# Kernel optimization log

Hardware: AMD Instinct MI355X
Metric: run time of the kernel (lower is better)

The kernel has to match this reference:

```python
import jax, jax.numpy as jnp
import numpy as np

B, N = 4, 1024
DIM, DEPTH, HEADS, DIM_HEAD, TCD = 512, 4, 8, 64, 512
HID = HEADS * DIM_HEAD  # 512
INNER = 4 * DIM         # 2048
MAX_REL = 32
N_REL = 2 * MAX_REL + 1  # 65
SCALE = DIM_HEAD ** -0.5
EPS = 1e-5


def setup_inputs() -> dict:
    key = jax.random.key(0)
    ks = jax.random.split(key, 16)
    s = 0.02
    inp = {
        "x": jax.random.normal(ks[0], (B, N, DIM), jnp.float32),
        "time": jax.random.normal(ks[1], (B, 1, TCD), jnp.float32),
        "seq_mask": jnp.ones((B, N), jnp.float32),
        "residue_index": jnp.tile(jnp.arange(N, dtype=jnp.int32)[None], (B, 1)),
        # relative positional encoding linear (65 -> heads)
        "relpos_w": jax.random.normal(ks[2], (N_REL, HEADS), jnp.float32) * s,
        "relpos_b": jnp.zeros((HEADS,), jnp.float32),
        # per-layer attention params (stacked over depth)
        "attn_norm_g": jnp.ones((DEPTH, DIM), jnp.float32),
        "attn_time_w": jax.random.normal(ks[3], (DEPTH, TCD, 2 * DIM), jnp.float32) * s,
        "attn_time_b": jnp.zeros((DEPTH, 2 * DIM), jnp.float32),
        "to_q_w": jax.random.normal(ks[4], (DEPTH, DIM, HID), jnp.float32) * s,
        "to_kv_w": jax.random.normal(ks[5], (DEPTH, DIM, 2 * HID), jnp.float32) * s,
        "to_out_w": jax.random.normal(ks[6], (DEPTH, HID, DIM), jnp.float32) * s,
        # per-layer feedforward params
        "ff_norm_g": jnp.ones((DEPTH, DIM), jnp.float32),
        "ff_time_w": jax.random.normal(ks[7], (DEPTH, TCD, 2 * INNER), jnp.float32) * s,
        "ff_time_b": jnp.zeros((DEPTH, 2 * INNER), jnp.float32),
        "ff_in_w": jax.random.normal(ks[8], (DEPTH, DIM, INNER), jnp.float32) * s,
        "ff_in_b": jnp.zeros((DEPTH, INNER), jnp.float32),
        "ff_out_w": jax.random.normal(ks[9], (DEPTH, INNER, DIM), jnp.float32) * s,
        "ff_out_b": jnp.zeros((DEPTH, DIM), jnp.float32),
    }
    return inp


def _ln(x, g):
    m = jnp.mean(x, axis=-1, keepdims=True)
    v = jnp.mean(jnp.square(x - m), axis=-1, keepdims=True)
    return (x - m) * jax.lax.rsqrt(v + EPS) * g


def _forward(x, time, seq_mask, residue_index, relpos_w, relpos_b,
             attn_norm_g, attn_time_w, attn_time_b, to_q_w, to_kv_w, to_out_w,
             ff_norm_g, ff_time_w, ff_time_b, ff_in_w, ff_in_b, ff_out_w, ff_out_b):
    # relative positional bias: [b, heads, i, j]
    d_ij = residue_index[:, :, None] - residue_index[:, None, :]
    idx = jnp.clip(d_ij, -MAX_REL, MAX_REL) + MAX_REL  # argmin over integer bins == clip
    bias = relpos_w[idx] + relpos_b                    # [b, i, j, h]
    bias = jnp.transpose(bias, (0, 3, 1, 2))           # [b, h, i, j]

    mask3 = seq_mask[..., None]                                       # [b, n, 1]
    pair_mask = seq_mask[:, None, :, None] * seq_mask[:, None, None, :]  # [b, 1, i, j]
    t_act = jax.nn.silu(time)                                         # [b, 1, tcd]

    x = x * mask3
    for d in range(DEPTH):
        # ---- attention block ----
        sc_sh = t_act @ attn_time_w[d] + attn_time_b[d]               # [b, 1, 2*dim]
        sc, sh = jnp.split(sc_sh, 2, axis=-1)
        xn = _ln(x, attn_norm_g[d]) * (sc + 1.0) + sh
        xn = xn * mask3
        q = (xn @ to_q_w[d]).reshape(B, N, HEADS, DIM_HEAD) * SCALE
        # NOTE: context = pre-norm x (faithful to original code)
        kv = (x @ to_kv_w[d]).reshape(B, N, 2, HEADS, DIM_HEAD)
        k, v = kv[:, :, 0], kv[:, :, 1]
        sim = jnp.einsum('bihd,bjhd->bhij', q, k) + bias
        sim = sim - (1.0 - pair_mask) * 1e6
        attn = jax.nn.softmax(sim, axis=-1)
        out = jnp.einsum('bhij,bjhd->bihd', attn, v).reshape(B, N, HID)
        out = (out @ to_out_w[d]) * mask3
        x = x + out
        # ---- feedforward block ----
        sc_sh = t_act @ ff_time_w[d] + ff_time_b[d]                   # [b, 1, 2*inner]
        sc, sh = jnp.split(sc_sh, 2, axis=-1)
        h = jax.nn.silu(_ln(x, ff_norm_g[d]) @ ff_in_w[d] + ff_in_b[d])
        h = h * (sc + 1.0) + sh
        x = x + (h @ ff_out_w[d] + ff_out_b[d])
        x = x * mask3
    return x


def reference(x, time, seq_mask, residue_index, relpos_w, relpos_b,
              attn_norm_g, attn_time_w, attn_time_b, to_q_w, to_kv_w, to_out_w,
              ff_norm_g, ff_time_w, ff_time_b, ff_in_w, ff_in_b, ff_out_w, ff_out_b):
    return _forward(x, time, seq_mask, residue_index, relpos_w, relpos_b,
                    attn_norm_g, attn_time_w, attn_time_b, to_q_w, to_kv_w, to_out_w,
                    ff_norm_g, ff_time_w, ff_time_b, ff_in_w, ff_in_b, ff_out_w, ff_out_b)
```

## Files before the change

kernel.cpp:

```cpp
#include <hip/hip_runtime.h>
#include <hip/hip_bf16.h>

constexpr int kB = 4, kN = 1024, kD = 512, kH = 8, kDh = 64, kT = 512;
constexpr int kHid = 512, kI = 2048, kRel = 65, kDepth = 4;
constexpr int kBN = kB * kN;

typedef short s16x8 __attribute__((ext_vector_type(8)));
typedef float f32x4 __attribute__((ext_vector_type(4)));

__device__ __forceinline__ float ldin(const void* p, long i, int isb) {
  if (isb) return __bfloat162float(((const __hip_bfloat16*)p)[i]);
  return ((const float*)p)[i];
}

__device__ __forceinline__ unsigned short bfbits(float v) {
  __hip_bfloat16 h = __float2bfloat16(v);
  return *(unsigned short*)&h;
}

__device__ __forceinline__ void gload16(const void* g, void* l) {
  __builtin_amdgcn_global_load_lds(
      (const __attribute__((address_space(1))) unsigned int*)g,
      (__attribute__((address_space(3))) unsigned int*)l, 16, 0, 0);
}

__global__ void k_detect(const void* __restrict__ x, int* __restrict__ flag) {
  const unsigned int* u = (const unsigned int*)x;
  unsigned int v = u[threadIdx.x];
  int e = (v >> 7) & 0xFF;
  int good = (e >= 100 && e <= 140) ? 1 : 0;
  unsigned long long m = __ballot(good);
  if (threadIdx.x == 0) flag[0] = (__popcll(m) >= 48) ? 1 : 0;
}

__global__ void k_xinit(const void* __restrict__ xin, const void* __restrict__ seqm,
                        float* __restrict__ x, __hip_bfloat16* __restrict__ xb,
                        const int* __restrict__ flag) {
  const int isb = *flag;
  const long base = ((long)blockIdx.x * 256 + threadIdx.x) * 8;
  const int row = (int)(base >> 9);
  const float mk = ldin(seqm, row, isb);
  __align__(16) unsigned short pk[8];
  #pragma unroll
  for (int j = 0; j < 8; j++) {
    float v = ldin(xin, base + j, isb) * mk;
    x[base + j] = v;
    pk[j] = bfbits(v);
  }
  *(uint4*)(xb + base) = *(const uint4*)pk;
}

__global__ __launch_bounds__(256) void k_timeproj_part(
    const void* __restrict__ timein,
    const void* __restrict__ atw, const void* __restrict__ ftw,
    float* __restrict__ part, const int* __restrict__ flag) {
  const int isb = *flag;
  __shared__ float T[kB * 64];
  const int d = blockIdx.z, kc = blockIdx.y;
  const int tt0 = kc * 64;
  {
    const int b = threadIdx.x >> 6, ttl = threadIdx.x & 63;
    const float tv = ldin(timein, (long)b * kT + tt0 + ttl, isb);
    T[b * 64 + ttl] = tv / (1.f + __expf(-tv));
  }
  __syncthreads();
  const int c = blockIdx.x * 256 + threadIdx.x;
  float a0 = 0, a1 = 0, a2 = 0, a3 = 0;
  if (c < 2 * kD) {
    const long wo = (long)d * kT * 2 * kD + (long)tt0 * 2 * kD + c;
    #pragma unroll 4
    for (int tt = 0; tt < 64; tt++) {
      const float w = ldin(atw, wo + (long)tt * 2 * kD, isb);
      a0 += T[0 * 64 + tt] * w; a1 += T[1 * 64 + tt] * w;
      a2 += T[2 * 64 + tt] * w; a3 += T[3 * 64 + tt] * w;
    }
  } else {
    const int c2 = c - 2 * kD;
    const long wo = (long)d * kT * 2 * kI + (long)tt0 * 2 * kI + c2;
    #pragma unroll 4
    for (int tt = 0; tt < 64; tt++) {
      const float w = ldin(ftw, wo + (long)tt * 2 * kI, isb);
      a0 += T[0 * 64 + tt] * w; a1 += T[1 * 64 + tt] * w;
      a2 += T[2 * 64 + tt] * w; a3 += T[3 * 64 + tt] * w;
    }
  }
  float* pp = part + ((long)(d * 8 + kc) * 4) * 5120 + c;
  pp[0] = a0; pp[5120] = a1; pp[2 * 5120] = a2; pp[3 * 5120] = a3;
}

__global__ __launch_bounds__(256) void k_timeproj_comb(
    const float* __restrict__ part,
    const void* __restrict__ atb, const void* __restrict__ ftb,
    float* __restrict__ ascsh, float* __restrict__ fscsh,
    const int* __restrict__ flag) {
  const int isb = *flag;
  const int d = blockIdx.y;
  const int c = blockIdx.x * 256 + threadIdx.x;
  float s[4] = {0, 0, 0, 0};
  #pragma unroll
  for (int kc = 0; kc < 8; kc++) {
    const float* pp = part + ((long)(d * 8 + kc) * 4) * 5120 + c;
    s[0] += pp[0]; s[1] += pp[5120]; s[2] += pp[2 * 5120]; s[3] += pp[3 * 5120];
  }
  if (c < 2 * kD) {
    const float bv = ldin(atb, (long)d * 2 * kD + c, isb);
    #pragma unroll
    for (int b = 0; b < 4; b++) ascsh[((long)d * kB + b) * 2 * kD + c] = s[b] + bv;
  } else {
    const int c2 = c - 2 * kD;
    const float bv = ldin(ftb, (long)d * 2 * kI + c2, isb);
    #pragma unroll
    for (int b = 0; b < 4; b++) fscsh[((long)d * kB + b) * 2 * kI + c2] = s[b] + bv;
  }
}

__global__ __launch_bounds__(256) void k_wtall(
    const void* __restrict__ wq, const void* __restrict__ wkv,
    const void* __restrict__ wo, const void* __restrict__ wfi,
    const void* __restrict__ wfo,
    __hip_bfloat16* __restrict__ wtq, __hip_bfloat16* __restrict__ wtkv,
    __hip_bfloat16* __restrict__ wto, __hip_bfloat16* __restrict__ wtfi,
    __hip_bfloat16* __restrict__ wtfo, const int* __restrict__ flag) {
  const int isb = *flag;
  __shared__ float T[64][65];
  const int bx = blockIdx.x;
  const void* W; __hip_bfloat16* Wt; int K, N, tl;
  if (bx < 256)       { W = wq;  Wt = wtq;  K = 512;  N = 512;  tl = bx; }
  else if (bx < 768)  { W = wkv; Wt = wtkv; K = 512;  N = 1024; tl = bx - 256; }
  else if (bx < 1024) { W = wo;  Wt = wto;  K = 512;  N = 512;  tl = bx - 768; }
  else if (bx < 2048) { W = wfi; Wt = wtfi; K = 512;  N = 2048; tl = bx - 1024; }
  else                { W = wfo; Wt = wtfo; K = 2048; N = 512;  tl = bx - 2048; }
  const int nx = N >> 6, nk = K >> 6;
  const int z = tl / (nx * nk);
  const int rem = tl % (nx * nk);
  const int k0 = (rem / nx) * 64, n0 = (rem % nx) * 64;
  const long ibase = (long)z * K * N;
  const long obase = (long)z * N * K;
  const int t = threadIdx.x;
  const int cn = t & 63, r4 = t >> 6;
  for (int rr = r4; rr < 64; rr += 4)
    T[rr][cn] = ldin(W, ibase + (long)(k0 + rr) * N + n0 + cn, isb);
  __syncthreads();
  for (int nn = r4; nn < 64; nn += 4)
    Wt[obase + (long)(n0 + nn) * K + k0 + cn] = __float2bfloat16(T[cn][nn]);
}

__global__ __launch_bounds__(256) void k_ln(
    const float* __restrict__ x, const void* __restrict__ g,
    const float* __restrict__ scsh, const void* __restrict__ seqm,
    __hip_bfloat16* __restrict__ xnb, int d, int domod, const int* __restrict__ flag) {
  const int isb = *flag;
  const int wid = threadIdx.x >> 6, lane = threadIdx.x & 63;
  const int row = blockIdx.x * 4 + wid;
  const int b = row >> 10;
  const float* xr = x + (long)row * kD + lane * 8;
  const float4 v0 = *(const float4*)xr;
  const float4 v1 = *(const float4*)(xr + 4);
  float v[8] = {v0.x, v0.y, v0.z, v0.w, v1.x, v1.y, v1.z, v1.w};
  float s = 0.f, s2 = 0.f;
  #pragma unroll
  for (int i = 0; i < 8; i++) { s += v[i]; s2 += v[i] * v[i]; }
  #pragma unroll
  for (int off = 1; off < 64; off <<= 1) { s += __shfl_xor(s, off); s2 += __shfl_xor(s2, off); }
  const float mean = s * (1.f / kD);
  const float var = fmaxf(s2 * (1.f / kD) - mean * mean, 0.f);
  const float rstd = rsqrtf(var + 1e-5f);
  float mk = 1.f;
  if (domod) mk = ldin(seqm, row, isb);
  __align__(16) unsigned short pk[8];
  #pragma unroll
  for (int i = 0; i < 8; i++) {
    const int cc = lane * 8 + i;
    float y = (v[i] - mean) * rstd * ldin(g, (long)d * kD + cc, isb);
    if (domod)
      y = (y * (scsh[(long)b * 2 * kD + cc] + 1.f) + scsh[(long)b * 2 * kD + kD + cc]) * mk;
    pk[i] = bfbits(y);
  }
  *(uint4*)(xnb + (long)row * kD + lane * 8) = *(const uint4*)pk;
}

template <int EPI, int BN>
__global__ __launch_bounds__(256) void k_mgemm(
    const __hip_bfloat16* __restrict__ A, const __hip_bfloat16* __restrict__ Wt,
    long woff, int K, int Nc,
    __hip_bfloat16* __restrict__ Cb,
    float* __restrict__ X, __hip_bfloat16* __restrict__ Xb,
    const void* __restrict__ bias, long boff,
    const float* __restrict__ scsh, const void* __restrict__ seqm,
    const int* __restrict__ flag) {
  constexpr int FN = BN / 32;
  const int isb = *flag;
  __shared__ __align__(16) short As[2][64 * 64];
  __shared__ __align__(16) short Bs[2][BN * 64];
  const int t = threadIdx.x;
  const int l = t & 63, wid = t >> 6;
  const int wm = wid & 1, wn = wid >> 1;
  const int lr = l >> 4, lc = l & 15;
  const int m0 = blockIdx.y * 64, n0 = blockIdx.x * BN;

  f32x4 acc[2][FN] = {};
  const int lrow8 = l >> 3;
  const int lchunk = (l & 7) ^ lrow8;
  const __hip_bfloat16* gA = A + (long)(m0 + wid * 8 + lrow8) * K + lchunk * 8;
  const __hip_bfloat16* gB = Wt + woff + (long)(n0 + wid * 8 + lrow8) * K + lchunk * 8;

  #pragma unroll
  for (int p = 0; p < 2; p++)
    gload16(gA + (long)p * 32 * K, &As[0][p * 2048 + wid * 512]);
  #pragma unroll
  for (int p = 0; p < FN; p++)
    gload16(gB + (long)p * 32 * K, &Bs[0][p * 2048 + wid * 512]);
  __syncthreads();

  const int nt = K >> 6;
  int cur = 0;
  for (int tt = 0; tt < nt; tt++) {
    if (tt + 1 < nt) {
      const int k0 = (tt + 1) * 64;
      #pragma unroll
      for (int p = 0; p < 2; p++)
        gload16(gA + (long)p * 32 * K + k0, &As[cur ^ 1][p * 2048 + wid * 512]);
      #pragma unroll
      for (int p = 0; p < FN; p++)
        gload16(gB + (long)p * 32 * K + k0, &Bs[cur ^ 1][p * 2048 + wid * 512]);
    }
    #pragma unroll
    for (int kk = 0; kk < 2; kk++) {
      s16x8 af[2], bf[FN];
      #pragma unroll
      for (int fm = 0; fm < 2; fm++) {
        const int r = wm * 32 + fm * 16 + lc;
        af[fm] = *(const s16x8*)&As[cur][r * 64 + (((kk * 4 + lr) ^ (r & 7)) * 8)];
      }
      #pragma unroll
      for (int fn = 0; fn < FN; fn++) {
        const int r = wn * (BN / 2) + fn * 16 + lc;
        bf[fn] = *(const s16x8*)&Bs[cur][r * 64 + (((kk * 4 + lr) ^ (r & 7)) * 8)];
      }
      #pragma unroll
      for (int fm = 0; fm < 2; fm++)
        #pragma unroll
        for (int fn = 0; fn < FN; fn++)
          acc[fm][fn] = __builtin_amdgcn_mfma_f32_16x16x32_bf16(af[fm], bf[fn], acc[fm][fn], 0, 0, 0);
    }
    __syncthreads();
    cur ^= 1;
  }

  #pragma unroll
  for (int fm = 0; fm < 2; fm++) {
    #pragma unroll
    for (int j = 0; j < 4; j++) {
      const int r = m0 + wm * 32 + fm * 16 + lr * 4 + j;
      const int bb = r >> 10;
      float mk = 1.f;
      if constexpr (EPI == 2 || EPI == 4) mk = ldin(seqm, r, isb);
      #pragma unroll
      for (int fn = 0; fn < FN; fn++) {
        const int cc = n0 + wn * (BN / 2) + fn * 16 + lc;
        const long off = (long)r * Nc + cc;
        float v = acc[fm][fn][j];
        if constexpr (EPI == 2) {
          X[off] += v * mk;
        } else if constexpr (EPI == 3) {
          v += ldin(bias, boff + cc, isb);
          v = v / (1.f + __expf(-v));
          v = v * (scsh[(long)bb * 2 * kI + cc] + 1.f) + scsh[(long)bb * 2 * kI + kI + cc];
          Cb[off] = __float2bfloat16(v);
        } else {
          v += ldin(bias, boff + cc, isb);
          const float nx = (X[off] + v) * mk;
          X[off] = nx;
          Xb[off] = __float2bfloat16(nx);
        }
      }
    }
  }
}

__global__ __launch_bounds__(256) void k_qkv(
    const __hip_bfloat16* __restrict__ xnb, const __hip_bfloat16* __restrict__ xb,
    const __hip_bfloat16* __restrict__ wtq, const __hip_bfloat16* __restrict__ wtkv,
    __hip_bfloat16* __restrict__ qbuf, __hip_bfloat16* __restrict__ kvb) {
  constexpr int K = kD;
  __shared__ __align__(16) short As[2][64 * 64];
  __shared__ __align__(16) short Bs[2][128 * 64];
  const int t = threadIdx.x;
  const int l = t & 63, wid = t >> 6;
  const int wm = wid & 1, wn = wid >> 1;
  const int lr = l >> 4, lc = l & 15;
  const int m0 = blockIdx.y * 64;

  const __hip_bfloat16* A; const __hip_bfloat16* Wt; __hip_bfloat16* C;
  int Nc, n0; float scale;
  if (blockIdx.x < 4) {
    A = xnb; Wt = wtq; C = qbuf; Nc = kHid; n0 = blockIdx.x * 128; scale = 0.125f;
  } else {
    A = xb; Wt = wtkv; C = kvb; Nc = 2 * kHid; n0 = (blockIdx.x - 4) * 128; scale = 1.f;
  }

  f32x4 acc[2][4] = {};
  const int lrow8 = l >> 3;
  const int lchunk = (l & 7) ^ lrow8;
  const __hip_bfloat16* gA = A + (long)(m0 + wid * 8 + lrow8) * K + lchunk * 8;
  const __hip_bfloat16* gB = Wt + (long)(n0 + wid * 8 + lrow8) * K + lchunk * 8;

  #pragma unroll
  for (int p = 0; p < 2; p++)
    gload16(gA + (long)p * 32 * K, &As[0][p * 2048 + wid * 512]);
  #pragma unroll
  for (int p = 0; p < 4; p++)
    gload16(gB + (long)p * 32 * K, &Bs[0][p * 2048 + wid * 512]);
  __syncthreads();

  const int nt = K >> 6;
  int cur = 0;
  for (int tt = 0; tt < nt; tt++) {
    if (tt + 1 < nt) {
      const int k0 = (tt + 1) * 64;
      #pragma unroll
      for (int p = 0; p < 2; p++)
        gload16(gA + (long)p * 32 * K + k0, &As[cur ^ 1][p * 2048 + wid * 512]);
      #pragma unroll
      for (int p = 0; p < 4; p++)
        gload16(gB + (long)p * 32 * K + k0, &Bs[cur ^ 1][p * 2048 + wid * 512]);
    }
    #pragma unroll
    for (int kk = 0; kk < 2; kk++) {
      s16x8 af[2], bf[4];
      #pragma unroll
      for (int fm = 0; fm < 2; fm++) {
        const int r = wm * 32 + fm * 16 + lc;
        af[fm] = *(const s16x8*)&As[cur][r * 64 + (((kk * 4 + lr) ^ (r & 7)) * 8)];
      }
      #pragma unroll
      for (int fn = 0; fn < 4; fn++) {
        const int r = wn * 64 + fn * 16 + lc;
        bf[fn] = *(const s16x8*)&Bs[cur][r * 64 + (((kk * 4 + lr) ^ (r & 7)) * 8)];
      }
      #pragma unroll
      for (int fm = 0; fm < 2; fm++)
        #pragma unroll
        for (int fn = 0; fn < 4; fn++)
          acc[fm][fn] = __builtin_amdgcn_mfma_f32_16x16x32_bf16(af[fm], bf[fn], acc[fm][fn], 0, 0, 0);
    }
    __syncthreads();
    cur ^= 1;
  }

  #pragma unroll
  for (int fm = 0; fm < 2; fm++)
    #pragma unroll
    for (int j = 0; j < 4; j++) {
      const int r = m0 + wm * 32 + fm * 16 + lr * 4 + j;
      #pragma unroll
      for (int fn = 0; fn < 4; fn++) {
        const int cc = n0 + wn * 64 + fn * 16 + lc;
        C[(long)r * Nc + cc] = __float2bfloat16(acc[fm][fn][j] * scale);
      }
    }
}

__global__ __launch_bounds__(256) void k_attn(
    const __hip_bfloat16* __restrict__ qb, const __hip_bfloat16* __restrict__ kvb,
    __hip_bfloat16* __restrict__ aob,
    const void* __restrict__ rpw, const void* __restrict__ rpb,
    const void* __restrict__ seqm, const int* __restrict__ ridx,
    const int* __restrict__ flag) {
  const int isb = *flag;
  const int t = threadIdx.x;
  const int bid = blockIdx.x;
  const int swz = (bid & 7) * 64 + (bid >> 3);
  const int x = swz & 15, h = (swz >> 4) & 7, b = swz >> 7;
  const int i0 = x * 64;

  __shared__ __align__(16) short Ks[2][64 * 64];
  __shared__ __align__(16) short Vt[2][64 * 72];
  __shared__ __align__(16) short Ps[4][16 * 72];
  __shared__ float biasw[kRel];
  __shared__ int riq[64];
  __shared__ float mkq[64];
  __shared__ int rik[2][64];
  __shared__ float mkk[2][64];

  const int l = t & 63, wid = t >> 6;
  const int g = l >> 4, li = l & 15;

  if (t < kRel) biasw[t] = ldin(rpw, (long)t * kH + h, isb) + ldin(rpb, h, isb);
  if (t < 64) { riq[t] = ridx[b * kN + i0 + t]; mkq[t] = ldin(seqm, b * kN + i0 + t, isb); }

  const __hip_bfloat16* qptr =
      qb + ((long)(b * kN + i0 + wid * 16 + li)) * kHid + h * kDh + g * 8;
  s16x8 aq[2];
  aq[0] = *(const s16x8*)qptr;
  aq[1] = *(const s16x8*)(qptr + 32);

  {
    #pragma unroll
    for (int p = 0; p < 2; p++) {
      const int j = p * 32 + wid * 8 + (l >> 3);
      const short* gk = (const short*)kvb + ((long)(b * kN + j)) * 1024 + h * 64 +
                        (((l & 7) ^ (l >> 3)) * 8);
      gload16(gk, &Ks[0][p * 2048 + wid * 512]);
    }
    const short* gv = (const short*)kvb + ((long)(b * kN + l)) * 1024 + 512 + h * 64 + wid * 16;
    s16x8 v0 = *(const s16x8*)gv;
    s16x8 v1 = *(const s16x8*)(gv + 8);
    #pragma unroll
    for (int dd = 0; dd < 8; dd++) {
      Vt[0][(wid * 16 + dd) * 72 + l] = v0[dd];
      Vt[0][(wid * 16 + 8 + dd) * 72 + l] = v1[dd];
    }
    if (t < 64) { rik[0][t] = ridx[b * kN + t]; mkk[0][t] = ldin(seqm, b * kN + t, isb); }
  }
  __syncthreads();

  float mkqv[4]; int riqv[4];
  #pragma unroll
  for (int r = 0; r < 4; r++) {
    riqv[r] = riq[wid * 16 + g * 4 + r];
    mkqv[r] = mkq[wid * 16 + g * 4 + r];
  }

  float m_run[4] = {-1e30f, -1e30f, -1e30f, -1e30f};
  float l_run[4] = {0.f, 0.f, 0.f, 0.f};
  f32x4 o[4] = {};

  constexpr int NT = kN / 64;
  int cur = 0;
  for (int tt = 0; tt < NT; tt++) {
    s16x8 nv0, nv1;
    int nri = 0; float nmk = 0.f;
    const bool have = (tt + 1) < NT;
    if (have) {
      const int j0n = (tt + 1) * 64;
      #pragma unroll
      for (int p = 0; p < 2; p++) {
        const int j = p * 32 + wid * 8 + (l >> 3);
        const short* gk = (const short*)kvb + ((long)(b * kN + j0n + j)) * 1024 + h * 64 +
                          (((l & 7) ^ (l >> 3)) * 8);
        gload16(gk, &Ks[cur ^ 1][p * 2048 + wid * 512]);
      }
      const short* gv =
          (const short*)kvb + ((long)(b * kN + j0n + l)) * 1024 + 512 + h * 64 + wid * 16;
      nv0 = *(const s16x8*)gv;
      nv1 = *(const s16x8*)(gv + 8);
      if (t < 64) { nri = ridx[b * kN + j0n + t]; nmk = ldin(seqm, b * kN + j0n + t, isb); }
    }

    f32x4 s[4] = {};
    __builtin_amdgcn_s_setprio(1);
    #pragma unroll
    for (int kc = 0; kc < 2; kc++) {
      #pragma unroll
      for (int fc = 0; fc < 4; fc++) {
        const int jl = fc * 16 + li;
        const s16x8 bk = *(const s16x8*)&Ks[cur][jl * 64 + ((kc * 32 + g * 8) ^ ((li & 7) * 8))];
        s[fc] = __builtin_amdgcn_mfma_f32_16x16x32_bf16(aq[kc], bk, s[fc], 0, 0, 0);
      }
    }
    __builtin_amdgcn_s_setprio(0);

    int rikv[4]; float mkkv[4];
    #pragma unroll
    for (int fc = 0; fc < 4; fc++) {
      rikv[fc] = rik[cur][fc * 16 + li];
      mkkv[fc] = mkk[cur][fc * 16 + li];
    }
    #pragma unroll
    for (int fc = 0; fc < 4; fc++) {
      #pragma unroll
      for (int r = 0; r < 4; r++) {
        int di = riqv[r] - rikv[fc];
        di = di < -32 ? -32 : (di > 32 ? 32 : di);
        s[fc][r] += biasw[di + 32] - (1.f - mkqv[r] * mkkv[fc]) * 1e6f;
      }
    }

    #pragma unroll
    for (int r = 0; r < 4; r++) {
      float mx = fmaxf(fmaxf(s[0][r], s[1][r]), fmaxf(s[2][r], s[3][r]));
      mx = fmaxf(mx, __shfl_xor(mx, 1));
      mx = fmaxf(mx, __shfl_xor(mx, 2));
      mx = fmaxf(mx, __shfl_xor(mx, 4));
      mx = fmaxf(mx, __shfl_xor(mx, 8));
      const float m_new = fmaxf(m_run[r], mx);
      const float e = __expf(m_run[r] - m_new);
      float ps = 0.f;
      #pragma unroll
      for (int fc = 0; fc < 4; fc++) {
        const float p = __expf(s[fc][r] - m_new);
        ps += p;
        Ps[wid][(g * 4 + r) * 72 + fc * 16 + li] = (short)bfbits(p);
      }
      ps += __shfl_xor(ps, 1);
      ps += __shfl_xor(ps, 2);
      ps += __shfl_xor(ps, 4);
      ps += __shfl_xor(ps, 8);
      l_run[r] = l_run[r] * e + ps;
      m_run[r] = m_new;
      o[0][r] *= e; o[1][r] *= e; o[2][r] *= e; o[3][r] *= e;
    }

    __builtin_amdgcn_s_setprio(1);
    #pragma unroll
    for (int kc = 0; kc < 2; kc++) {
      const s16x8 pa = *(const s16x8*)&Ps[wid][li * 72 + kc * 32 + g * 8];
      #pragma unroll
      for (int fd = 0; fd < 4; fd++) {
        const s16x8 bv = *(const s16x8*)&Vt[cur][(fd * 16 + li) * 72 + kc * 32 + g * 8];
        o[fd] = __builtin_amdgcn_mfma_f32_16x16x32_bf16(pa, bv, o[fd], 0, 0, 0);
      }
    }
    __builtin_amdgcn_s_setprio(0);

    if (have) {
      #pragma unroll
      for (int dd = 0; dd < 8; dd++) {
        Vt[cur ^ 1][(wid * 16 + dd) * 72 + l] = nv0[dd];
        Vt[cur ^ 1][(wid * 16 + 8 + dd) * 72 + l] = nv1[dd];
      }
      if (t < 64) { rik[cur ^ 1][t] = nri; mkk[cur ^ 1][t] = nmk; }
    }
    __syncthreads();
    cur ^= 1;
  }

  float inv[4];
  #pragma unroll
  for (int r = 0; r < 4; r++) inv[r] = 1.f / l_run[r];
  #pragma unroll
  for (int fd = 0; fd < 4; fd++) {
    #pragma unroll
    for (int r = 0; r < 4; r++) {
      const long off =
          ((long)(b * kN + i0 + wid * 16 + g * 4 + r)) * kHid + h * kDh + fd * 16 + li;
      aob[off] = __float2bfloat16(o[fd][r] * inv[r]);
    }
  }
}

__global__ void k_out(const float* __restrict__ x, void* __restrict__ out,
                      const int* __restrict__ flag) {
  const int i = blockIdx.x * 256 + threadIdx.x;
  if (*flag) ((__hip_bfloat16*)out)[i] = __float2bfloat16(x[i]);
  else ((float*)out)[i] = x[i];
}

extern "C" void kernel_launch(void* const* d_in, const int* in_sizes, int n_in,
                              void* d_out, int out_size, void* d_ws, size_t ws_size,
                              hipStream_t stream) {
  const void* xin  = d_in[0];
  const void* timein = d_in[1];
  const void* seqm = d_in[2];
  const int*  ridx = (const int*)d_in[3];
  const void* rpw  = d_in[4];
  const void* rpb  = d_in[5];
  const void* ang  = d_in[6];
  const void* atw  = d_in[7];
  const void* atb  = d_in[8];
  const void* wq   = d_in[9];
  const void* wkv  = d_in[10];
  const void* wo   = d_in[11];
  const void* fng  = d_in[12];
  const void* ftw  = d_in[13];
  const void* ftb  = d_in[14];
  const void* wfi  = d_in[15];
  const void* bfi  = d_in[16];
  const void* wfo  = d_in[17];
  const void* bfo  = d_in[18];

  float* ws = (float*)d_ws;
  float* x     = ws;
  float* ascsh = ws + 2097152;
  float* fscsh = ws + 2113536;
  float* part  = ws + 2179072;
  int*   flag  = (int*)(ws + 2834432);
  __hip_bfloat16* bfb = (__hip_bfloat16*)(ws + 2834496);
  __hip_bfloat16* xnb  = bfb;
  __hip_bfloat16* xb   = bfb + 2097152;
  __hip_bfloat16* aob  = bfb + 4194304;
  __hip_bfloat16* hb   = bfb + 6291456;
  __hip_bfloat16* qbuf = bfb + 14680064;
  __hip_bfloat16* kvb  = bfb + 16777216;
  __hip_bfloat16* wtq  = bfb + 20971520;
  __hip_bfloat16* wtkv = bfb + 22020096;
  __hip_bfloat16* wto  = bfb + 24117248;
  __hip_bfloat16* wtfi = bfb + 25165824;
  __hip_bfloat16* wtfo = bfb + 29360128;

  k_detect<<<1, 64, 0, stream>>>(xin, flag);
  k_xinit<<<kBN * kD / 2048, 256, 0, stream>>>(xin, seqm, x, xb, flag);
  k_timeproj_part<<<dim3(20, 8, kDepth), 256, 0, stream>>>(timein, atw, ftw, part, flag);
  k_timeproj_comb<<<dim3(20, kDepth), 256, 0, stream>>>(part, atb, ftb, ascsh, fscsh, flag);
  k_wtall<<<3072, 256, 0, stream>>>(wq, wkv, wo, wfi, wfo, wtq, wtkv, wto, wtfi, wtfo, flag);

  for (int d = 0; d < kDepth; ++d) {
    k_ln<<<kBN / 4, 256, 0, stream>>>(x, ang, ascsh + (long)d * kB * 2 * kD, seqm, xnb, d, 1, flag);
    k_qkv<<<dim3(12, kBN / 64), 256, 0, stream>>>(
        xnb, xb, wtq + (long)d * kD * kHid, wtkv + (long)d * kD * 2 * kHid, qbuf, kvb);
    k_attn<<<512, 256, 0, stream>>>(qbuf, kvb, aob, rpw, rpb, seqm, ridx, flag);
    k_mgemm<2, 64><<<dim3(kD / 64, kBN / 64), 256, 0, stream>>>(
        aob, wto, (long)d * kHid * kD, kHid, kD, nullptr, x, nullptr,
        nullptr, 0, nullptr, seqm, flag);
    k_ln<<<kBN / 4, 256, 0, stream>>>(x, fng, nullptr, seqm, xnb, d, 0, flag);
    k_mgemm<3, 128><<<dim3(kI / 128, kBN / 64), 256, 0, stream>>>(
        xnb, wtfi, (long)d * kD * kI, kD, kI, hb, nullptr, nullptr,
        bfi, (long)d * kI, fscsh + (long)d * kB * 2 * kI, nullptr, flag);
    k_mgemm<4, 64><<<dim3(kD / 64, kBN / 64), 256, 0, stream>>>(
        hb, wtfo, (long)d * kI * kD, kI, kD, nullptr, x, xb,
        bfo, (long)d * kD, nullptr, seqm, flag);
  }
  k_out<<<kBN * kD / 256, 256, 0, stream>>>(x, d_out, flag);
}
```

Before: 792.3 us.

## Split attention over key halves with a combine kernel, shrink GEMM tiles

```diff
diff --git a/kernel.cpp b/kernel.cpp
--- a/kernel.cpp
+++ b/kernel.cpp
@@ -284,7 +284,7 @@
     __hip_bfloat16* __restrict__ qbuf, __hip_bfloat16* __restrict__ kvb) {
   constexpr int K = kD;
   __shared__ __align__(16) short As[2][64 * 64];
-  __shared__ __align__(16) short Bs[2][128 * 64];
+  __shared__ __align__(16) short Bs[2][64 * 64];
   const int t = threadIdx.x;
   const int l = t & 63, wid = t >> 6;
   const int wm = wid & 1, wn = wid >> 1;
@@ -293,24 +293,23 @@
 
   const __hip_bfloat16* A; const __hip_bfloat16* Wt; __hip_bfloat16* C;
   int Nc, n0; float scale;
-  if (blockIdx.x < 4) {
-    A = xnb; Wt = wtq; C = qbuf; Nc = kHid; n0 = blockIdx.x * 128; scale = 0.125f;
+  if (blockIdx.x < 8) {
+    A = xnb; Wt = wtq; C = qbuf; Nc = kHid; n0 = blockIdx.x * 64; scale = 0.125f;
   } else {
-    A = xb; Wt = wtkv; C = kvb; Nc = 2 * kHid; n0 = (blockIdx.x - 4) * 128; scale = 1.f;
-  }
-
-  f32x4 acc[2][4] = {};
+    A = xb; Wt = wtkv; C = kvb; Nc = 2 * kHid; n0 = (blockIdx.x - 8) * 64; scale = 1.f;
+  }
+
+  f32x4 acc[2][2] = {};
   const int lrow8 = l >> 3;
   const int lchunk = (l & 7) ^ lrow8;
   const __hip_bfloat16* gA = A + (long)(m0 + wid * 8 + lrow8) * K + lchunk * 8;
   const __hip_bfloat16* gB = Wt + (long)(n0 + wid * 8 + lrow8) * K + lchunk * 8;
 
   #pragma unroll
-  for (int p = 0; p < 2; p++)
+  for (int p = 0; p < 2; p++) {
     gload16(gA + (long)p * 32 * K, &As[0][p * 2048 + wid * 512]);
-  #pragma unroll
-  for (int p = 0; p < 4; p++)
     gload16(gB + (long)p * 32 * K, &Bs[0][p * 2048 + wid * 512]);
+  }
   __syncthreads();
 
   const int nt = K >> 6;
@@ -319,29 +318,28 @@
     if (tt + 1 < nt) {
       const int k0 = (tt + 1) * 64;
       #pragma unroll
-      for (int p = 0; p < 2; p++)
+      for (int p = 0; p < 2; p++) {
         gload16(gA + (long)p * 32 * K + k0, &As[cur ^ 1][p * 2048 + wid * 512]);
-      #pragma unroll
-      for (int p = 0; p < 4; p++)
         gload16(gB + (long)p * 32 * K + k0, &Bs[cur ^ 1][p * 2048 + wid * 512]);
+      }
     }
     #pragma unroll
     for (int kk = 0; kk < 2; kk++) {
-      s16x8 af[2], bf[4];
+      s16x8 af[2], bf[2];
       #pragma unroll
       for (int fm = 0; fm < 2; fm++) {
         const int r = wm * 32 + fm * 16 + lc;
         af[fm] = *(const s16x8*)&As[cur][r * 64 + (((kk * 4 + lr) ^ (r & 7)) * 8)];
       }
       #pragma unroll
-      for (int fn = 0; fn < 4; fn++) {
-        const int r = wn * 64 + fn * 16 + lc;
+      for (int fn = 0; fn < 2; fn++) {
+        const int r = wn * 32 + fn * 16 + lc;
         bf[fn] = *(const s16x8*)&Bs[cur][r * 64 + (((kk * 4 + lr) ^ (r & 7)) * 8)];
       }
       #pragma unroll
       for (int fm = 0; fm < 2; fm++)
         #pragma unroll
-        for (int fn = 0; fn < 4; fn++)
+        for (int fn = 0; fn < 2; fn++)
           acc[fm][fn] = __builtin_amdgcn_mfma_f32_16x16x32_bf16(af[fm], bf[fn], acc[fm][fn], 0, 0, 0);
     }
     __syncthreads();
@@ -354,16 +352,16 @@
     for (int j = 0; j < 4; j++) {
       const int r = m0 + wm * 32 + fm * 16 + lr * 4 + j;
       #pragma unroll
-      for (int fn = 0; fn < 4; fn++) {
-        const int cc = n0 + wn * 64 + fn * 16 + lc;
+      for (int fn = 0; fn < 2; fn++) {
+        const int cc = n0 + wn * 32 + fn * 16 + lc;
         C[(long)r * Nc + cc] = __float2bfloat16(acc[fm][fn][j] * scale);
       }
     }
 }
 
-__global__ __launch_bounds__(256) void k_attn(
+__global__ __launch_bounds__(512) void k_attn(
     const __hip_bfloat16* __restrict__ qb, const __hip_bfloat16* __restrict__ kvb,
-    __hip_bfloat16* __restrict__ aob,
+    float* __restrict__ opart, float* __restrict__ mpart, float* __restrict__ lpart,
     const void* __restrict__ rpw, const void* __restrict__ rpb,
     const void* __restrict__ seqm, const int* __restrict__ ridx,
     const int* __restrict__ flag) {
@@ -371,15 +369,16 @@
   const int t = threadIdx.x;
   const int bid = blockIdx.x;
   const int swz = (bid & 7) * 64 + (bid >> 3);
-  const int x = swz & 15, h = (swz >> 4) & 7, b = swz >> 7;
-  const int i0 = x * 64;
+  const int jh = swz & 1, x = (swz >> 1) & 7, h = (swz >> 4) & 7, b = swz >> 7;
+  const int i0 = x * 128;
+  const int jbase = jh * 512;
 
   __shared__ __align__(16) short Ks[2][64 * 64];
   __shared__ __align__(16) short Vt[2][64 * 72];
-  __shared__ __align__(16) short Ps[4][16 * 72];
+  __shared__ __align__(16) short Ps[8][16 * 72];
   __shared__ float biasw[kRel];
-  __shared__ int riq[64];
-  __shared__ float mkq[64];
+  __shared__ int riq[128];
+  __shared__ float mkq[128];
   __shared__ int rik[2][64];
   __shared__ float mkk[2][64];
 
@@ -387,7 +386,7 @@
   const int g = l >> 4, li = l & 15;
 
   if (t < kRel) biasw[t] = ldin(rpw, (long)t * kH + h, isb) + ldin(rpb, h, isb);
-  if (t < 64) { riq[t] = ridx[b * kN + i0 + t]; mkq[t] = ldin(seqm, b * kN + i0 + t, isb); }
+  if (t < 128) { riq[t] = ridx[b * kN + i0 + t]; mkq[t] = ldin(seqm, b * kN + i0 + t, isb); }
 
   const __hip_bfloat16* qptr =
       qb + ((long)(b * kN + i0 + wid * 16 + li)) * kHid + h * kDh + g * 8;
@@ -396,22 +395,19 @@
   aq[1] = *(const s16x8*)(qptr + 32);
 
   {
-    #pragma unroll
-    for (int p = 0; p < 2; p++) {
-      const int j = p * 32 + wid * 8 + (l >> 3);
-      const short* gk = (const short*)kvb + ((long)(b * kN + j)) * 1024 + h * 64 +
-                        (((l & 7) ^ (l >> 3)) * 8);
-      gload16(gk, &Ks[0][p * 2048 + wid * 512]);
-    }
-    const short* gv = (const short*)kvb + ((long)(b * kN + l)) * 1024 + 512 + h * 64 + wid * 16;
+    const int j = wid * 8 + (l >> 3);
+    const short* gk = (const short*)kvb + ((long)(b * kN + jbase + j)) * 1024 + h * 64 +
+                      (((l & 7) ^ (l >> 3)) * 8);
+    gload16(gk, &Ks[0][wid * 512]);
+    const short* gv =
+        (const short*)kvb + ((long)(b * kN + jbase + l)) * 1024 + 512 + h * 64 + wid * 8;
     s16x8 v0 = *(const s16x8*)gv;
-    s16x8 v1 = *(const s16x8*)(gv + 8);
-    #pragma unroll
-    for (int dd = 0; dd < 8; dd++) {
-      Vt[0][(wid * 16 + dd) * 72 + l] = v0[dd];
-      Vt[0][(wid * 16 + 8 + dd) * 72 + l] = v1[dd];
-    }
-    if (t < 64) { rik[0][t] = ridx[b * kN + t]; mkk[0][t] = ldin(seqm, b * kN + t, isb); }
+    #pragma unroll
+    for (int dd = 0; dd < 8; dd++) Vt[0][(wid * 8 + dd) * 72 + l] = v0[dd];
+    if (t < 64) {
+      rik[0][t] = ridx[b * kN + jbase + t];
+      mkk[0][t] = ldin(seqm, b * kN + jbase + t, isb);
+    }
   }
   __syncthreads();
 
@@ -426,25 +422,21 @@
   float l_run[4] = {0.f, 0.f, 0.f, 0.f};
   f32x4 o[4] = {};
 
-  constexpr int NT = kN / 64;
+  constexpr int NT = 8;
   int cur = 0;
   for (int tt = 0; tt < NT; tt++) {
-    s16x8 nv0, nv1;
+    s16x8 nv0;
     int nri = 0; float nmk = 0.f;
     const bool have = (tt + 1) < NT;
     if (have) {
-      const int j0n = (tt + 1) * 64;
-      #pragma unroll
-      for (int p = 0; p < 2; p++) {
-        const int j = p * 32 + wid * 8 + (l >> 3);
-        const short* gk = (const short*)kvb + ((long)(b * kN + j0n + j)) * 1024 + h * 64 +
-                          (((l & 7) ^ (l >> 3)) * 8);
-        gload16(gk, &Ks[cur ^ 1][p * 2048 + wid * 512]);
-      }
+      const int j0n = jbase + (tt + 1) * 64;
+      const int j = wid * 8 + (l >> 3);
+      const short* gk = (const short*)kvb + ((long)(b * kN + j0n + j)) * 1024 + h * 64 +
+                        (((l & 7) ^ (l >> 3)) * 8);
+      gload16(gk, &Ks[cur ^ 1][wid * 512]);
       const short* gv =
-          (const short*)kvb + ((long)(b * kN + j0n + l)) * 1024 + 512 + h * 64 + wid * 16;
+          (const short*)kvb + ((long)(b * kN + j0n + l)) * 1024 + 512 + h * 64 + wid * 8;
       nv0 = *(const s16x8*)gv;
-      nv1 = *(const s16x8*)(gv + 8);
       if (t < 64) { nri = ridx[b * kN + j0n + t]; nmk = ldin(seqm, b * kN + j0n + t, isb); }
     }
 
@@ -516,28 +508,60 @@
 
     if (have) {
       #pragma unroll
-      for (int dd = 0; dd < 8; dd++) {
-        Vt[cur ^ 1][(wid * 16 + dd) * 72 + l] = nv0[dd];
-        Vt[cur ^ 1][(wid * 16 + 8 + dd) * 72 + l] = nv1[dd];
-      }
+      for (int dd = 0; dd < 8; dd++) Vt[cur ^ 1][(wid * 8 + dd) * 72 + l] = nv0[dd];
       if (t < 64) { rik[cur ^ 1][t] = nri; mkk[cur ^ 1][t] = nmk; }
     }
     __syncthreads();
     cur ^= 1;
   }
 
-  float inv[4];
-  #pragma unroll
-  for (int r = 0; r < 4; r++) inv[r] = 1.f / l_run[r];
   #pragma unroll
   for (int fd = 0; fd < 4; fd++) {
     #pragma unroll
     for (int r = 0; r < 4; r++) {
       const long off =
           ((long)(b * kN + i0 + wid * 16 + g * 4 + r)) * kHid + h * kDh + fd * 16 + li;
-      aob[off] = __float2bfloat16(o[fd][r] * inv[r]);
-    }
-  }
+      opart[(long)jh * 2097152 + off] = o[fd][r];
+    }
+  }
+  if (li == 0) {
+    #pragma unroll
+    for (int r = 0; r < 4; r++) {
+      const int row = i0 + wid * 16 + g * 4 + r;
+      const int idx = (b * kN + row) * 8 + h;
+      mpart[jh * 32768 + idx] = m_run[r];
+      lpart[jh * 32768 + idx] = l_run[r];
+    }
+  }
+}
+
+__global__ __launch_bounds__(256) void k_acomb(
+    const float* __restrict__ opart, const float* __restrict__ mpart,
+    const float* __restrict__ lpart, __hip_bfloat16* __restrict__ aob) {
+  const long e = ((long)blockIdx.x * 256 + threadIdx.x) * 8;
+  const int h = (int)((e >> 6) & 7);
+  const int row = (int)(e >> 9);
+  const int idx = row * 8 + h;
+  const float m0 = mpart[idx], m1 = mpart[32768 + idx];
+  const float l0 = lpart[idx], l1 = lpart[32768 + idx];
+  const float mm = fmaxf(m0, m1);
+  const float e0 = __expf(m0 - mm), e1 = __expf(m1 - mm);
+  const float den = fmaxf(e0 * l0 + e1 * l1, 1e-30f);
+  const float s0 = e0 / den, s1 = e1 / den;
+  const float4 a0 = *(const float4*)(opart + e);
+  const float4 a1 = *(const float4*)(opart + e + 4);
+  const float4 b0 = *(const float4*)(opart + 2097152 + e);
+  const float4 b1 = *(const float4*)(opart + 2097152 + e + 4);
+  __align__(16) unsigned short pk[8];
+  pk[0] = bfbits(a0.x * s0 + b0.x * s1);
+  pk[1] = bfbits(a0.y * s0 + b0.y * s1);
+  pk[2] = bfbits(a0.z * s0 + b0.z * s1);
+  pk[3] = bfbits(a0.w * s0 + b0.w * s1);
+  pk[4] = bfbits(a1.x * s0 + b1.x * s1);
+  pk[5] = bfbits(a1.y * s0 + b1.y * s1);
+  pk[6] = bfbits(a1.z * s0 + b1.z * s1);
+  pk[7] = bfbits(a1.w * s0 + b1.w * s1);
+  *(uint4*)(aob + e) = *(const uint4*)pk;
 }
 
 __global__ void k_out(const float* __restrict__ x, void* __restrict__ out,
@@ -588,6 +612,9 @@
   __hip_bfloat16* wto  = bfb + 24117248;
   __hip_bfloat16* wtfi = bfb + 25165824;
   __hip_bfloat16* wtfo = bfb + 29360128;
+  float* opart = (float*)hb;
+  float* mpart = part;
+  float* lpart = part + 65536;
 
   k_detect<<<1, 64, 0, stream>>>(xin, flag);
   k_xinit<<<kBN * kD / 2048, 256, 0, stream>>>(xin, seqm, x, xb, flag);
@@ -597,14 +624,15 @@
 
   for (int d = 0; d < kDepth; ++d) {
     k_ln<<<kBN / 4, 256, 0, stream>>>(x, ang, ascsh + (long)d * kB * 2 * kD, seqm, xnb, d, 1, flag);
-    k_qkv<<<dim3(12, kBN / 64), 256, 0, stream>>>(
+    k_qkv<<<dim3(24, kBN / 64), 256, 0, stream>>>(
         xnb, xb, wtq + (long)d * kD * kHid, wtkv + (long)d * kD * 2 * kHid, qbuf, kvb);
-    k_attn<<<512, 256, 0, stream>>>(qbuf, kvb, aob, rpw, rpb, seqm, ridx, flag);
+    k_attn<<<512, 512, 0, stream>>>(qbuf, kvb, opart, mpart, lpart, rpw, rpb, seqm, ridx, flag);
+    k_acomb<<<1024, 256, 0, stream>>>(opart, mpart, lpart, aob);
     k_mgemm<2, 64><<<dim3(kD / 64, kBN / 64), 256, 0, stream>>>(
         aob, wto, (long)d * kHid * kD, kHid, kD, nullptr, x, nullptr,
         nullptr, 0, nullptr, seqm, flag);
     k_ln<<<kBN / 4, 256, 0, stream>>>(x, fng, nullptr, seqm, xnb, d, 0, flag);
-    k_mgemm<3, 128><<<dim3(kI / 128, kBN / 64), 256, 0, stream>>>(
+    k_mgemm<3, 64><<<dim3(kI / 64, kBN / 64), 256, 0, stream>>>(
         xnb, wtfi, (long)d * kD * kI, kD, kI, hb, nullptr, nullptr,
         bfi, (long)d * kI, fscsh + (long)d * kB * 2 * kI, nullptr, flag);
     k_mgemm<4, 64><<<dim3(kD / 64, kBN / 64), 256, 0, stream>>>(
```

New measurement: 768.5 us. -3.0%, faster.
